# Kernel tuning notes

Hardware: AMD Instinct MI355X
Metric: run time of the kernel (lower is better)

The kernel has to match this reference:

```python
import jax, jax.numpy as jnp
import numpy as np

K = 64  # nodes kept per graph (SortPooling k)

def setup_inputs() -> dict:
    key = jax.random.key(0)
    N, D = 131072, 256  # 256 graphs x 512 nodes
    feat = jax.random.normal(key, (N, D), dtype=jnp.float32)
    return {"feat": feat, "num_graphs": 256}

def reference(feat, num_graphs):
    # feat: (N, D) node features; batched graph of `num_graphs` equal-sized graphs
    N, D = feat.shape
    n = N // num_graphs  # nodes per graph
    # 1) sort each node's feature vector ascending along feature dim (tf.sort(feat, -1))
    feat_s = jnp.sort(feat, axis=-1)
    # 2) segmented top-k: rank nodes within each graph by the LAST feature value
    #    (sortby=-1), descending, and keep k nodes (DGL topk_nodes semantics)
    fb = feat_s.reshape(num_graphs, n, D)  # (B, n, D)
    scores = fb[:, :, -1]                  # (B, n) = max of each sorted row
    _, idx = jax.lax.top_k(scores, K)      # descending order, (B, k)
    topk = jnp.take_along_axis(fb, idx[:, :, None], axis=1)  # (B, k, D)
    # 3) flatten to (B, k*D)
    return topk.reshape(num_graphs, K * D)
```

## Files before the change

### kernel.cpp

```cpp
#include <hip/hip_runtime.h>
#include <hip/hip_bf16.h>

#define NROWS   131072
#define D       256
#define NGRAPH  256
#define NPG     512
#define KSEL    64

__global__ __launch_bounds__(256) void row_max_kernel(const float* __restrict__ feat,
                                                      float* __restrict__ scores) {
    const int wave = (blockIdx.x * 256 + threadIdx.x) >> 6;
    const int lane = threadIdx.x & 63;
    const int row0 = wave * 4;

    const float4* p = reinterpret_cast<const float4*>(feat) + (size_t)row0 * 64 + lane;
    const float4 a = p[0], b = p[64], c = p[128], d = p[192];

    float m0 = fmaxf(fmaxf(a.x, a.y), fmaxf(a.z, a.w));
    float m1 = fmaxf(fmaxf(b.x, b.y), fmaxf(b.z, b.w));
    float m2 = fmaxf(fmaxf(c.x, c.y), fmaxf(c.z, c.w));
    float m3 = fmaxf(fmaxf(d.x, d.y), fmaxf(d.z, d.w));

#pragma unroll
    for (int off = 32; off > 0; off >>= 1) {
        m0 = fmaxf(m0, __shfl_xor(m0, off));
        m1 = fmaxf(m1, __shfl_xor(m1, off));
        m2 = fmaxf(m2, __shfl_xor(m2, off));
        m3 = fmaxf(m3, __shfl_xor(m3, off));
    }
    if (lane < 4) {
        const float m = (lane == 0) ? m0 : (lane == 1) ? m1 : (lane == 2) ? m2 : m3;
        scores[row0 + lane] = m;
    }
}

__global__ __launch_bounds__(512) void topk_kernel(const float* __restrict__ scores,
                                                   int* __restrict__ idx_out) {
    __shared__ float s[NPG];
    __shared__ int   id[NPG];
    const int g = blockIdx.x;
    const int t = threadIdx.x;

    s[t]  = scores[g * NPG + t];
    id[t] = t;
    __syncthreads();

    for (int k = 2; k <= NPG; k <<= 1) {
        for (int j = k >> 1; j > 0; j >>= 1) {
            const int ixj = t ^ j;
            if (ixj > t) {
                const float s1 = s[t], s2 = s[ixj];
                const int   i1 = id[t], i2 = id[ixj];
                const bool before = (s1 > s2) || (s1 == s2 && i1 < i2);
                const bool up     = ((t & k) == 0);
                if (up ? !before : before) {
                    s[t] = s2; s[ixj] = s1;
                    id[t] = i2; id[ixj] = i1;
                }
            }
            __syncthreads();
        }
    }

    if (t < KSEL) idx_out[g * KSEL + t] = g * NPG + id[t];
}

__global__ __launch_bounds__(256) void sort_row_kernel(const float* __restrict__ feat,
                                                       const int* __restrict__ idx,
                                                       float* __restrict__ out) {
    const int wv   = threadIdx.x >> 6;
    const int lane = threadIdx.x & 63;
    const int b    = blockIdx.x * 4 + wv;
    const int row  = idx[b];

    const float* src = feat + (size_t)row * D;
    float v[4];
#pragma unroll
    for (int r = 0; r < 4; ++r) v[r] = src[r * 64 + lane];

#pragma unroll
    for (int k = 2; k <= 256; k <<= 1) {
#pragma unroll
        for (int j = k >> 1; j > 0; j >>= 1) {
            if (j >= 64) {
                const int rb = j >> 6;
#pragma unroll
                for (int r = 0; r < 4; ++r) {
                    if ((r & rb) == 0) {
                        const int rp = r | rb;
                        const bool up = (k == 256) ? true : ((r & 2) == 0);
                        const float mn = fminf(v[r], v[rp]);
                        const float mx = fmaxf(v[r], v[rp]);
                        v[r]  = up ? mn : mx;
                        v[rp] = up ? mx : mn;
                    }
                }
            } else {
#pragma unroll
                for (int r = 0; r < 4; ++r) {
                    const float o = __shfl_xor(v[r], j);
                    bool up;
                    if      (k <= 32)  up = ((lane & k) == 0);
                    else if (k == 64)  up = ((r & 1) == 0);
                    else if (k == 128) up = ((r & 2) == 0);
                    else               up = true;
                    const bool lower = ((lane & j) == 0);
                    const float mn = fminf(v[r], o);
                    const float mx = fmaxf(v[r], o);
                    v[r] = (up == lower) ? mn : mx;
                }
            }
        }
    }

    float* dst = out + (size_t)b * D;
#pragma unroll
    for (int r = 0; r < 4; ++r) dst[r * 64 + lane] = v[r];
}

extern "C" void kernel_launch(void* const* d_in, const int* in_sizes, int n_in,
                              void* d_out, int out_size, void* d_ws, size_t ws_size,
                              hipStream_t stream) {
    const float* feat = (const float*)d_in[0];
    float* out = (float*)d_out;

    float* scores = (float*)d_ws;
    int*   idx    = (int*)((char*)d_ws + (size_t)NROWS * sizeof(float));

    row_max_kernel<<<NROWS / 16, 256, 0, stream>>>(feat, scores);

    topk_kernel<<<NGRAPH, NPG, 0, stream>>>(scores, idx);

    sort_row_kernel<<<NGRAPH * KSEL / 4, 256, 0, stream>>>(feat, idx, out);
}
```

Measured before the change: 225.3 us.

## Replace shared-memory bitonic top-k with single-wave register bitonic sort on packed keys

The per-graph top-k selection moves from a 512-thread shared-memory bitonic sort, which needs a barrier after every step, to one 64-lane wave that holds 8 keys per lane in registers. Each score and its index are packed into a 64-bit orderable key (flipped float bits, inverted index so ties keep the lower index), and compare-exchanges use register swaps or cross-lane shuffles. This removes the shared-memory traffic and block barriers, but each graph now runs on a single wave with 64-bit compares, and only 256 small blocks are launched.

```diff
diff --git a/kernel.cpp b/kernel.cpp
--- a/kernel.cpp
+++ b/kernel.cpp
@@ -34,35 +34,59 @@
     }
 }
 
-__global__ __launch_bounds__(512) void topk_kernel(const float* __restrict__ scores,
-                                                   int* __restrict__ idx_out) {
-    __shared__ float s[NPG];
-    __shared__ int   id[NPG];
-    const int g = blockIdx.x;
-    const int t = threadIdx.x;
+__global__ __launch_bounds__(64) void topk_kernel(const float* __restrict__ scores,
+                                                  int* __restrict__ idx_out) {
+    const int g    = blockIdx.x;
+    const int lane = threadIdx.x & 63;
 
-    s[t]  = scores[g * NPG + t];
-    id[t] = t;
-    __syncthreads();
+    const float* s = scores + (size_t)g * NPG;
+    unsigned long long key[8];
+#pragma unroll
+    for (int r = 0; r < 8; ++r) {
+        const int i = r * 64 + lane;
+        const unsigned int fb = __float_as_uint(s[i]);
+        const unsigned int u  = (fb & 0x80000000u) ? ~fb : (fb | 0x80000000u);
+        key[r] = ((unsigned long long)u << 32) | (unsigned int)(~i);
+    }
 
-    for (int k = 2; k <= NPG; k <<= 1) {
+#pragma unroll
+    for (int k = 2; k <= 512; k <<= 1) {
+#pragma unroll
         for (int j = k >> 1; j > 0; j >>= 1) {
-            const int ixj = t ^ j;
-            if (ixj > t) {
-                const float s1 = s[t], s2 = s[ixj];
-                const int   i1 = id[t], i2 = id[ixj];
-                const bool before = (s1 > s2) || (s1 == s2 && i1 < i2);
-                const bool up     = ((t & k) == 0);
-                if (up ? !before : before) {
-                    s[t] = s2; s[ixj] = s1;
-                    id[t] = i2; id[ixj] = i1;
+            if (j >= 64) {
+                const int rb = j >> 6;
+#pragma unroll
+                for (int r = 0; r < 8; ++r) {
+                    if ((r & rb) == 0) {
+                        const int rp = r | rb;
+                        const bool up = (k == 512) ? true : ((r & (k >> 6)) == 0);
+                        const unsigned long long lo = (key[r] < key[rp]) ? key[r] : key[rp];
+                        const unsigned long long hi = (key[r] < key[rp]) ? key[rp] : key[r];
+                        key[r]  = up ? hi : lo;
+                        key[rp] = up ? lo : hi;
+                    }
+                }
+            } else {
+#pragma unroll
+                for (int r = 0; r < 8; ++r) {
+                    const unsigned long long o = __shfl_xor(key[r], j);
+                    bool up;
+                    if      (k <= 32)  up = ((lane & k) == 0);
+                    else if (k == 64)  up = ((r & 1) == 0);
+                    else if (k == 128) up = ((r & 2) == 0);
+                    else if (k == 256) up = ((r & 4) == 0);
+                    else               up = true;
+                    const bool lower = ((lane & j) == 0);
+                    const unsigned long long mn = (key[r] < o) ? key[r] : o;
+                    const unsigned long long mx = (key[r] < o) ? o : key[r];
+                    key[r] = (up == lower) ? mx : mn;
                 }
             }
-            __syncthreads();
         }
     }
 
-    if (t < KSEL) idx_out[g * KSEL + t] = g * NPG + id[t];
+    const int local = (int)(~(unsigned int)(key[0] & 0xFFFFFFFFull));
+    idx_out[g * KSEL + lane] = g * NPG + local;
 }
 
 __global__ __launch_bounds__(256) void sort_row_kernel(const float* __restrict__ feat,
@@ -129,7 +153,7 @@
 
     row_max_kernel<<<NROWS / 16, 256, 0, stream>>>(feat, scores);
 
-    topk_kernel<<<NGRAPH, NPG, 0, stream>>>(scores, idx);
+    topk_kernel<<<NGRAPH, 64, 0, stream>>>(scores, idx);
 
     sort_row_kernel<<<NGRAPH * KSEL / 4, 256, 0, stream>>>(feat, idx, out);
 }
```

Result: no change. 227.0 us (+0.7%).
